# Kernel optimization log

Measured on AMD Instinct MI355X. Metric: run time of the kernel, lower is better.

The kernel has to match this reference:

```python
import jax, jax.numpy as jnp
import numpy as np

N_NODES = 50000
N_EDGES = 1600000
SLOPE = 0.01  # torch leaky_relu default negative_slope


def _lrelu(x):
    return jnp.where(x >= 0, x, SLOPE * x)


def _graph_conv(x, edge_index, w_rel, b_rel, w_root):
    # PyG GraphConv (aggr='add'): out_i = W_rel @ sum_{j->i} x_j + b_rel + W_root @ x_i
    src, dst = edge_index[0], edge_index[1]
    agg = jax.ops.segment_sum(x[src], dst, num_segments=x.shape[0])  # [N, F_in]
    return agg @ w_rel.T + b_rel + x @ w_root.T


def setup_inputs() -> dict:
    key = jax.random.key(0)
    ks = jax.random.split(key, 12)

    def glorot(k, shape):
        fan_in = shape[-1]
        return jax.random.normal(k, shape, dtype=jnp.float32) / np.sqrt(fan_in)

    x = jax.random.normal(ks[0], (N_NODES, 2048), dtype=jnp.float32)
    edge_index = jax.random.randint(ks[1], (2, N_EDGES), 0, N_NODES, dtype=jnp.int64)

    return {
        "x": x,
        "edge_index": edge_index,
        "lin1_w": glorot(ks[2], (128, 2048)),
        "lin1_b": jnp.zeros((128,), jnp.float32),
        "conv1_w_rel": glorot(ks[3], (64, 128)),
        "conv1_b_rel": jnp.zeros((64,), jnp.float32),
        "conv1_w_root": glorot(ks[4], (64, 128)),
        "conv4_w_rel": glorot(ks[5], (32, 64)),
        "conv4_b_rel": jnp.zeros((32,), jnp.float32),
        "conv4_w_root": glorot(ks[6], (32, 64)),
        "pos_w": glorot(ks[7], (3, 32)),
        "pos_b": jnp.zeros((3,), jnp.float32),
    }


def reference(x, edge_index, lin1_w, lin1_b, conv1_w_rel, conv1_b_rel,
              conv1_w_root, conv4_w_rel, conv4_b_rel, conv4_w_root,
              pos_w, pos_b):
    # dropout layers are identity at inference
    h = _lrelu(x @ lin1_w.T + lin1_b)                                  # [N, 128]
    h = _lrelu(_graph_conv(h, edge_index, conv1_w_rel, conv1_b_rel, conv1_w_root))  # [N, 64]
    h = _lrelu(_graph_conv(h, edge_index, conv4_w_rel, conv4_b_rel, conv4_w_root))  # [N, 32]
    position = h @ pos_w.T + pos_b                                     # [N, 3]
    return position
```

## Files before the change

kernel.cpp:

```cpp
#include <hip/hip_runtime.h>

#define N_NODES 50000
#define N_EDGES 1600000
#define LIN_BLOCKS 782
#define HIST_BLOCKS 1024

typedef __attribute__((ext_vector_type(4))) float f32x4;
typedef __attribute__((ext_vector_type(8))) short bf16x8;
typedef unsigned short u16;

__device__ __forceinline__ float lrelu(float x) { return x >= 0.f ? x : 0.01f * x; }

__device__ __forceinline__ u16 f2bf(float f) {
    union { float f; unsigned u; } v; v.f = f;
    unsigned u = v.u;
    u += 0x7fffu + ((u >> 16) & 1u);
    return (u16)(u >> 16);
}

__device__ __forceinline__ float bf2f(u16 v) {
    union { unsigned u; float f; } x; x.u = ((unsigned)v) << 16; return x.f;
}

__device__ __forceinline__ bf16x8 cvt8(float4 a, float4 b) {
    bf16x8 r;
    r[0] = (short)f2bf(a.x); r[1] = (short)f2bf(a.y);
    r[2] = (short)f2bf(a.z); r[3] = (short)f2bf(a.w);
    r[4] = (short)f2bf(b.x); r[5] = (short)f2bf(b.y);
    r[6] = (short)f2bf(b.z); r[7] = (short)f2bf(b.w);
    return r;
}

__launch_bounds__(256)
__global__ void k_prep(const float* __restrict__ W1,
                       const float* __restrict__ W2a, const float* __restrict__ W2b,
                       const float* __restrict__ W3a, const float* __restrict__ W3b,
                       u16* __restrict__ wf1, u16* __restrict__ wf2, u16* __restrict__ wf3,
                       const int* __restrict__ ei, int* __restrict__ deg)
{
    const int b = blockIdx.x;
    if (b < 1024) {
        int i = b * 256 + threadIdx.x;
        int e = i & 7, lane = (i >> 3) & 63, nf = (i >> 9) & 7, ks = i >> 12;
        int n = nf * 16 + (lane & 15);
        int k = ks * 32 + 8 * (lane >> 4) + e;
        wf1[i] = f2bf(W1[(size_t)n * 2048 + k]);
    } else if (b < 1088) {
        int i = (b - 1024) * 256 + threadIdx.x;
        int e = i & 7, lane = (i >> 3) & 63, nf = (i >> 9) & 7, ks = i >> 12;
        int n = nf * 16 + (lane & 15);
        int k = ks * 32 + 8 * (lane >> 4) + e;
        float v = (n < 64) ? W2a[(size_t)n * 128 + k] : W2b[(size_t)(n - 64) * 128 + k];
        wf2[i] = f2bf(v);
    } else if (b < 1104) {
        int i = (b - 1088) * 256 + threadIdx.x;
        int e = i & 7, lane = (i >> 3) & 63, nf = (i >> 9) & 3, ks = i >> 11;
        int n = nf * 16 + (lane & 15);
        int k = ks * 32 + 8 * (lane >> 4) + e;
        float v = (n < 32) ? W3a[(size_t)n * 64 + k] : W3b[(size_t)(n - 32) * 64 + k];
        wf3[i] = f2bf(v);
    } else {
        for (int e = (b - 1104) * 256 + threadIdx.x; e < N_EDGES; e += HIST_BLOCKS * 256)
            atomicAdd(deg + ei[N_EDGES + e], 1);
    }
}

__device__ __forceinline__ void compute_step(const char* slot, int lane, int wave,
                                             f32x4 acc[2][4])
{
    const int lrow = lane & 15;
    const int k16 = lane >> 4;
    const int nfb = (wave >> 1) << 2;
    const int rb = (wave & 1) << 5;

    bf16x8 af[2];
#pragma unroll
    for (int st = 0; st < 2; st++) {
        const int row = rb + st * 16 + lrow;
        af[st] = *(const bf16x8*)(slot + row * 64 + ((k16 ^ (row & 3)) << 4));
    }
    bf16x8 bf[4];
#pragma unroll
    for (int j = 0; j < 4; j++)
        bf[j] = *(const bf16x8*)(slot + 4096 + (nfb + j) * 1024 + lane * 16);

    __builtin_amdgcn_s_setprio(1);
#pragma unroll
    for (int st = 0; st < 2; st++)
#pragma unroll
        for (int j = 0; j < 4; j++)
            acc[st][j] = __builtin_amdgcn_mfma_f32_16x16x32_bf16(af[st], bf[j], acc[st][j], 0, 0, 0);
    __builtin_amdgcn_s_setprio(0);
}

__launch_bounds__(256, 4)
__global__ void k_linf(const float* __restrict__ X, const u16* __restrict__ Wf1,
                       const u16* __restrict__ Wf2,
                       const float* __restrict__ Bv, const float* __restrict__ brel,
                       u16* __restrict__ t1, float* __restrict__ acc1,
                       const int* __restrict__ ei, int* __restrict__ cur,
                       int* __restrict__ csr)
{
    __shared__ __align__(16) char lds[2][12288];

    const int t = threadIdx.x, wave = t >> 6, lane = t & 63;
    const int lrow = lane & 15, lgrp = lane >> 4;
    const int m0 = blockIdx.x * 64;

    const int arow_l = t >> 2, kq = t & 3;
    int grow = m0 + arow_l; if (grow >= N_NODES) grow = N_NODES - 1;
    const float4* ap = (const float4*)(X + (size_t)grow * 2048);
    const bf16x8* bp = (const bf16x8*)Wf1;
    const int awr = arow_l * 64 + ((kq ^ (arow_l & 3)) << 4);
    const int bwr = 4096 + t * 32;

    f32x4 acc[2][4];
#pragma unroll
    for (int st = 0; st < 2; st++)
#pragma unroll
        for (int j = 0; j < 4; j++) acc[st][j] = (f32x4)0.f;

    float4 cA0 = ap[kq * 2], cA1 = ap[kq * 2 + 1];
    bf16x8 cB0 = bp[t * 2], cB1 = bp[t * 2 + 1];
    float4 nA0 = ap[8 + kq * 2], nA1 = ap[8 + kq * 2 + 1];
    bf16x8 nB0 = bp[512 + t * 2], nB1 = bp[512 + t * 2 + 1];
    *(bf16x8*)(lds[0] + awr) = cvt8(cA0, cA1);
    *(bf16x8*)(lds[0] + bwr) = cB0;
    *(bf16x8*)(lds[0] + bwr + 16) = cB1;
    asm volatile("s_waitcnt lgkmcnt(0)" ::: "memory");
    __builtin_amdgcn_s_barrier();
    __builtin_amdgcn_sched_barrier(0);

#pragma unroll 2
    for (int s = 0; s < 62; s++) {
        float4 fA0 = ap[(s + 2) * 8 + kq * 2], fA1 = ap[(s + 2) * 8 + kq * 2 + 1];
        bf16x8 fB0 = bp[(s + 2) * 512 + t * 2], fB1 = bp[(s + 2) * 512 + t * 2 + 1];

        compute_step(lds[s & 1], lane, wave, acc);
        __builtin_amdgcn_s_barrier();
        __builtin_amdgcn_sched_barrier(0);

        char* wslot = lds[(s + 1) & 1];
        *(bf16x8*)(wslot + awr) = cvt8(nA0, nA1);
        *(bf16x8*)(wslot + bwr) = nB0;
        *(bf16x8*)(wslot + bwr + 16) = nB1;
        asm volatile("s_waitcnt lgkmcnt(0)" ::: "memory");
        __builtin_amdgcn_s_barrier();
        __builtin_amdgcn_sched_barrier(0);

        nA0 = fA0; nA1 = fA1; nB0 = fB0; nB1 = fB1;
    }
    compute_step(lds[0], lane, wave, acc);
    __builtin_amdgcn_s_barrier();
    __builtin_amdgcn_sched_barrier(0);
    *(bf16x8*)(lds[1] + awr) = cvt8(nA0, nA1);
    *(bf16x8*)(lds[1] + bwr) = nB0;
    *(bf16x8*)(lds[1] + bwr + 16) = nB1;
    asm volatile("s_waitcnt lgkmcnt(0)" ::: "memory");
    __builtin_amdgcn_s_barrier();
    __builtin_amdgcn_sched_barrier(0);
    compute_step(lds[1], lane, wave, acc);
    __builtin_amdgcn_s_barrier();
    __builtin_amdgcn_sched_barrier(0);

    u16* hl = (u16*)&lds[0][0];
    {
        const int nfb = (wave >> 1) << 2, rb = (wave & 1) << 5;
#pragma unroll
        for (int st = 0; st < 2; st++) {
#pragma unroll
            for (int j = 0; j < 4; j++) {
                const int col = nfb * 16 + j * 16 + lrow;
                const float bias = Bv[col];
#pragma unroll
                for (int r = 0; r < 4; r++) {
                    const int row = rb + st * 16 + lgrp * 4 + r;
                    hl[row * 128 + (((col >> 3) ^ (row & 7)) << 3) + (col & 7)] =
                        f2bf(lrelu(acc[st][j][r] + bias));
                }
            }
        }
    }
    asm volatile("s_waitcnt lgkmcnt(0)" ::: "memory");
    __builtin_amdgcn_s_barrier();
    __builtin_amdgcn_sched_barrier(0);

    bf16x8 af2[4];
    {
        const int row = wave * 16 + lrow;
#pragma unroll
        for (int ks = 0; ks < 4; ks++) {
            const int chunk = ((ks << 2) + lgrp) ^ (row & 7);
            af2[ks] = *(const bf16x8*)(hl + row * 128 + (chunk << 3));
        }
    }
    f32x4 dacc[8];
#pragma unroll
    for (int i = 0; i < 8; i++) dacc[i] = (f32x4)0.f;
    const u16* bp2 = Wf2 + lane * 8;
#pragma unroll
    for (int ks = 0; ks < 4; ks++) {
#pragma unroll
        for (int nf = 0; nf < 8; nf++) {
            bf16x8 bf = *(const bf16x8*)(bp2 + ks * 4096 + nf * 512);
            dacc[nf] = __builtin_amdgcn_mfma_f32_16x16x32_bf16(af2[ks], bf, dacc[nf], 0, 0, 0);
        }
    }

    const int rbase = m0 + wave * 16 + lgrp * 4;
#pragma unroll
    for (int nf = 0; nf < 8; nf++) {
        const int col = nf * 16 + lrow;
#pragma unroll
        for (int r = 0; r < 4; r++) {
            const int row = rbase + r;
            if (row < N_NODES) {
                if (col < 64) t1[(size_t)row * 64 + col] = f2bf(dacc[nf][r]);
                else          acc1[(size_t)row * 64 + (col - 64)] = dacc[nf][r] + brel[col - 64];
            }
        }
    }

    for (int e = blockIdx.x * 256 + t; e < N_EDGES; e += LIN_BLOCKS * 256) {
        const int dst = ei[N_EDGES + e];
        const int p = atomicAdd(cur + dst, 1);
        csr[p] = ei[e];
    }
}

__launch_bounds__(256, 2)
__global__ void k_dualf2(const float* __restrict__ A, const u16* __restrict__ Wf,
                         const float* __restrict__ brel,
                         u16* __restrict__ t2, float* __restrict__ acc2)
{
    const int t = threadIdx.x, wave = t >> 6, lane = t & 63;
    const int lrow = lane & 15, lgrp = lane >> 4;
    const int arow = blockIdx.x * 64 + wave * 16 + lrow;
    const float* ap = A + (size_t)(arow < N_NODES ? arow : 0) * 64 + 8 * lgrp;
    const u16* bp = Wf + lane * 8;

    float4 a00 = *(const float4*)(ap + 0);
    float4 a01 = *(const float4*)(ap + 4);
    float4 a10 = *(const float4*)(ap + 32);
    float4 a11 = *(const float4*)(ap + 36);

    f32x4 acc[4];
#pragma unroll
    for (int i = 0; i < 4; i++) acc[i] = (f32x4)0.f;

    a00.x = lrelu(a00.x); a00.y = lrelu(a00.y); a00.z = lrelu(a00.z); a00.w = lrelu(a00.w);
    a01.x = lrelu(a01.x); a01.y = lrelu(a01.y); a01.z = lrelu(a01.z); a01.w = lrelu(a01.w);
    bf16x8 af0 = cvt8(a00, a01);
    a10.x = lrelu(a10.x); a10.y = lrelu(a10.y); a10.z = lrelu(a10.z); a10.w = lrelu(a10.w);
    a11.x = lrelu(a11.x); a11.y = lrelu(a11.y); a11.z = lrelu(a11.z); a11.w = lrelu(a11.w);
    bf16x8 af1 = cvt8(a10, a11);

#pragma unroll
    for (int nf = 0; nf < 4; nf++) {
        bf16x8 b0 = *(const bf16x8*)(bp + nf * 512);
        bf16x8 b1 = *(const bf16x8*)(bp + 2048 + nf * 512);
        acc[nf] = __builtin_amdgcn_mfma_f32_16x16x32_bf16(af0, b0, acc[nf], 0, 0, 0);
        acc[nf] = __builtin_amdgcn_mfma_f32_16x16x32_bf16(af1, b1, acc[nf], 0, 0, 0);
    }

    const int rbase = blockIdx.x * 64 + wave * 16 + lgrp * 4;
#pragma unroll
    for (int nf = 0; nf < 4; nf++) {
        const int col = nf * 16 + lrow;
#pragma unroll
        for (int r = 0; r < 4; r++) {
            const int row = rbase + r;
            if (row < N_NODES) {
                if (col < 32) t2[(size_t)row * 32 + col] = f2bf(acc[nf][r]);
                else          acc2[(size_t)row * 32 + (col - 32)] = acc[nf][r] + brel[col - 32];
            }
        }
    }
}

__launch_bounds__(256)
__global__ void k_scan1(const int* __restrict__ deg, int* __restrict__ tmp,
                        int* __restrict__ bsum)
{
    __shared__ int sm[256];
    const int tid = threadIdx.x;
    const int i = blockIdx.x * 256 + tid;
    int d = (i < N_NODES) ? deg[i] : 0;
    sm[tid] = d;
    __syncthreads();
#pragma unroll
    for (int off = 1; off < 256; off <<= 1) {
        int v = (tid >= off) ? sm[tid - off] : 0;
        __syncthreads();
        sm[tid] += v;
        __syncthreads();
    }
    if (i < N_NODES) tmp[i] = sm[tid];
    if (tid == 255) bsum[blockIdx.x] = sm[255];
}

__launch_bounds__(256)
__global__ void k_scan2p(const int* __restrict__ bsum, int* __restrict__ boff, int nb)
{
    __shared__ int sm[256];
    const int tid = threadIdx.x;
    int v = (tid < nb) ? bsum[tid] : 0;
    sm[tid] = v;
    __syncthreads();
#pragma unroll
    for (int off = 1; off < 256; off <<= 1) {
        int u = (tid >= off) ? sm[tid - off] : 0;
        __syncthreads();
        sm[tid] += u;
        __syncthreads();
    }
    if (tid < nb) boff[tid] = sm[tid] - v;
}

__launch_bounds__(256)
__global__ void k_scan3(const int* __restrict__ tmp, const int* __restrict__ boff,
                        const int* __restrict__ deg, int* __restrict__ ro,
                        int* __restrict__ cur)
{
    const int i = blockIdx.x * 256 + threadIdx.x;
    if (i < N_NODES) {
        int incl = tmp[i] + boff[i >> 8];
        ro[i + 1] = incl;
        cur[i] = incl - deg[i];
    }
    if (i == 0) ro[0] = 0;
}

__launch_bounds__(256)
__global__ void k_gather64(const int* __restrict__ ro, const int* __restrict__ csr,
                           const u16* __restrict__ t, float* __restrict__ acc)
{
    const int wid = (blockIdx.x << 2) | (threadIdx.x >> 6);
    if (wid >= N_NODES) return;
    const int lane = threadIdx.x & 63;
    const int s = ro[wid], e = ro[wid + 1];
    float a = acc[(size_t)wid * 64 + lane];
    int i = s;
    for (; i + 8 <= e; i += 8) {
        int s0 = csr[i], s1 = csr[i + 1], s2 = csr[i + 2], s3 = csr[i + 3];
        int s4 = csr[i + 4], s5 = csr[i + 5], s6 = csr[i + 6], s7 = csr[i + 7];
        u16 v0 = t[(size_t)s0 * 64 + lane], v1 = t[(size_t)s1 * 64 + lane];
        u16 v2 = t[(size_t)s2 * 64 + lane], v3 = t[(size_t)s3 * 64 + lane];
        u16 v4 = t[(size_t)s4 * 64 + lane], v5 = t[(size_t)s5 * 64 + lane];
        u16 v6 = t[(size_t)s6 * 64 + lane], v7 = t[(size_t)s7 * 64 + lane];
        a += bf2f(v0); a += bf2f(v1); a += bf2f(v2); a += bf2f(v3);
        a += bf2f(v4); a += bf2f(v5); a += bf2f(v6); a += bf2f(v7);
    }
    for (; i < e; ++i) a += bf2f(t[(size_t)csr[i] * 64 + lane]);
    acc[(size_t)wid * 64 + lane] = a;
}

__launch_bounds__(256)
__global__ void k_gpos(const int* __restrict__ ro, const int* __restrict__ csr,
                       const u16* __restrict__ t, const float* __restrict__ acc2,
                       const float* __restrict__ PW, const float* __restrict__ PB,
                       float* __restrict__ out)
{
    const int wid = (blockIdx.x << 2) | (threadIdx.x >> 6);
    if (wid >= N_NODES) return;
    const int lane = threadIdx.x & 63;
    const int half = lane >> 5, f = lane & 31;
    const int s = ro[wid], e = ro[wid + 1];
    float a = 0.f;
    int i = s;
    for (; i + 8 <= e; i += 8) {
        int s0 = csr[i + half], s1 = csr[i + 2 + half];
        int s2 = csr[i + 4 + half], s3 = csr[i + 6 + half];
        u16 v0 = t[(size_t)s0 * 32 + f], v1 = t[(size_t)s1 * 32 + f];
        u16 v2 = t[(size_t)s2 * 32 + f], v3 = t[(size_t)s3 * 32 + f];
        a += bf2f(v0); a += bf2f(v1); a += bf2f(v2); a += bf2f(v3);
    }
    for (; i < e; i += 2) {
        int idx = i + half;
        if (idx < e) a += bf2f(t[(size_t)csr[idx] * 32 + f]);
    }
    a += __shfl_xor(a, 32, 64);

    float v = lrelu(acc2[(size_t)wid * 32 + f] + a);
    float p0 = v * PW[f], p1 = v * PW[32 + f], p2 = v * PW[64 + f];
#pragma unroll
    for (int off = 16; off >= 1; off >>= 1) {
        p0 += __shfl_xor(p0, off, 64);
        p1 += __shfl_xor(p1, off, 64);
        p2 += __shfl_xor(p2, off, 64);
    }
    if (lane == 0) {
        out[(size_t)wid * 3 + 0] = p0 + PB[0];
        out[(size_t)wid * 3 + 1] = p1 + PB[1];
        out[(size_t)wid * 3 + 2] = p2 + PB[2];
    }
}

extern "C" void kernel_launch(void* const* d_in, const int* in_sizes, int n_in,
                              void* d_out, int out_size, void* d_ws, size_t ws_size,
                              hipStream_t stream)
{
    const float* x        = (const float*)d_in[0];
    const int*   ei       = (const int*)d_in[1];
    const float* lin1_w   = (const float*)d_in[2];
    const float* lin1_b   = (const float*)d_in[3];
    const float* c1_wrel  = (const float*)d_in[4];
    const float* c1_brel  = (const float*)d_in[5];
    const float* c1_wroot = (const float*)d_in[6];
    const float* c4_wrel  = (const float*)d_in[7];
    const float* c4_brel  = (const float*)d_in[8];
    const float* c4_wroot = (const float*)d_in[9];
    const float* pos_w    = (const float*)d_in[10];
    const float* pos_b    = (const float*)d_in[11];
    float* out = (float*)d_out;

    char* base = (char*)d_ws;
    u16*   t1b  = (u16*)base;
    float* acc1 = (float*)(base + 6400000);
    u16*   t2b  = (u16*)(base + 19200000);
    float* acc2 = (float*)(base + 22400000);
    u16*   wf1  = (u16*)(base + 28800000);
    u16*   wf2  = wf1 + 262144;
    u16*   wf3  = wf2 + 16384;
    int*   ibase = (int*)(wf3 + 4096);
    const int NPAD = ((N_NODES + 255) / 256) * 256;
    int* deg  = ibase;
    int* tmp  = deg  + NPAD;
    int* ro   = tmp  + NPAD;
    int* cur  = ro   + NPAD;
    int* bsum = cur  + NPAD;
    int* boff = bsum + 256;
    int* csr  = boff + 256;
    const int NB = (N_NODES + 255) / 256;

    hipMemsetAsync(deg, 0, (size_t)NPAD * sizeof(int), stream);
    hipLaunchKernelGGL(k_prep, dim3(1104 + HIST_BLOCKS), dim3(256), 0, stream,
                       lin1_w, c1_wrel, c1_wroot, c4_wrel, c4_wroot,
                       wf1, wf2, wf3, ei, deg);
    hipLaunchKernelGGL(k_scan1, dim3(NB), dim3(256), 0, stream, deg, tmp, bsum);
    hipLaunchKernelGGL(k_scan2p, dim3(1), dim3(256), 0, stream, bsum, boff, NB);
    hipLaunchKernelGGL(k_scan3, dim3(NB), dim3(256), 0, stream, tmp, boff, deg, ro, cur);

    hipLaunchKernelGGL(k_linf, dim3(LIN_BLOCKS), dim3(256), 0, stream,
                       x, wf1, wf2, lin1_b, c1_brel, t1b, acc1, ei, cur, csr);
    hipLaunchKernelGGL(k_gather64, dim3((N_NODES + 3) / 4), dim3(256), 0, stream,
                       ro, csr, t1b, acc1);
    hipLaunchKernelGGL(k_dualf2, dim3((N_NODES + 63) / 64), dim3(256), 0, stream,
                       acc1, wf3, c4_brel, t2b, acc2);
    hipLaunchKernelGGL(k_gpos, dim3((N_NODES + 3) / 4), dim3(256), 0, stream,
                       ro, csr, t2b, acc2, pos_w, pos_b, out);
}
```

Baseline: 361.4 us.

## Enlarge lin1 GEMM tile to 128 rows and split CSR build into separate kernels

The first fused linear kernel now processes 128 rows per block with 512 threads. The shared weight tile is reused across twice as many rows, and each thread loads half as much of B. The CSR fill loop and the degree histogram move out of the GEMM and prep kernels into standalone k_fill and k_hist kernels, and the deg memset is folded into k_prep. The s_setprio hints around the MFMAs are dropped. In exchange, the atomic CSR fill no longer overlaps with the GEMM, and the pipeline gains extra kernel launches.

```diff
diff --git a/kernel.cpp b/kernel.cpp
--- a/kernel.cpp
+++ b/kernel.cpp
@@ -2,12 +2,12 @@
 
 #define N_NODES 50000
 #define N_EDGES 1600000
-#define LIN_BLOCKS 782
-#define HIST_BLOCKS 1024
 
 typedef __attribute__((ext_vector_type(4))) float f32x4;
 typedef __attribute__((ext_vector_type(8))) short bf16x8;
 typedef unsigned short u16;
+
+#define ABYTES 8192
 
 __device__ __forceinline__ float lrelu(float x) { return x >= 0.f ? x : 0.01f * x; }
 
@@ -36,7 +36,7 @@
                        const float* __restrict__ W2a, const float* __restrict__ W2b,
                        const float* __restrict__ W3a, const float* __restrict__ W3b,
                        u16* __restrict__ wf1, u16* __restrict__ wf2, u16* __restrict__ wf3,
-                       const int* __restrict__ ei, int* __restrict__ deg)
+                       int* __restrict__ deg)
 {
     const int b = blockIdx.x;
     if (b < 1024) {
@@ -60,9 +60,17 @@
         float v = (n < 32) ? W3a[(size_t)n * 64 + k] : W3b[(size_t)(n - 32) * 64 + k];
         wf3[i] = f2bf(v);
     } else {
-        for (int e = (b - 1104) * 256 + threadIdx.x; e < N_EDGES; e += HIST_BLOCKS * 256)
-            atomicAdd(deg + ei[N_EDGES + e], 1);
-    }
+        int i = (b - 1104) * 256 + threadIdx.x;
+        if (i < N_NODES) deg[i] = 0;
+    }
+}
+
+__launch_bounds__(256)
+__global__ void k_hist(const int* __restrict__ ei, int* __restrict__ deg)
+{
+    const int stride = gridDim.x * 256;
+    for (int e = blockIdx.x * 256 + threadIdx.x; e < N_EDGES; e += stride)
+        atomicAdd(deg + ei[N_EDGES + e], 1);
 }
 
 __device__ __forceinline__ void compute_step(const char* slot, int lane, int wave,
@@ -70,49 +78,45 @@
 {
     const int lrow = lane & 15;
     const int k16 = lane >> 4;
-    const int nfb = (wave >> 1) << 2;
-    const int rb = (wave & 1) << 5;
+    const int rs = wave >> 1;
+    const int ch = wave & 1;
 
     bf16x8 af[2];
 #pragma unroll
     for (int st = 0; st < 2; st++) {
-        const int row = rb + st * 16 + lrow;
+        const int row = rs * 32 + st * 16 + lrow;
         af[st] = *(const bf16x8*)(slot + row * 64 + ((k16 ^ (row & 3)) << 4));
     }
     bf16x8 bf[4];
 #pragma unroll
     for (int j = 0; j < 4; j++)
-        bf[j] = *(const bf16x8*)(slot + 4096 + (nfb + j) * 1024 + lane * 16);
-
-    __builtin_amdgcn_s_setprio(1);
+        bf[j] = *(const bf16x8*)(slot + ABYTES + (ch * 4 + j) * 1024 + lane * 16);
+
 #pragma unroll
     for (int st = 0; st < 2; st++)
 #pragma unroll
         for (int j = 0; j < 4; j++)
             acc[st][j] = __builtin_amdgcn_mfma_f32_16x16x32_bf16(af[st], bf[j], acc[st][j], 0, 0, 0);
-    __builtin_amdgcn_s_setprio(0);
-}
-
-__launch_bounds__(256, 4)
+}
+
+__launch_bounds__(512, 4)
 __global__ void k_linf(const float* __restrict__ X, const u16* __restrict__ Wf1,
                        const u16* __restrict__ Wf2,
                        const float* __restrict__ Bv, const float* __restrict__ brel,
-                       u16* __restrict__ t1, float* __restrict__ acc1,
-                       const int* __restrict__ ei, int* __restrict__ cur,
-                       int* __restrict__ csr)
-{
-    __shared__ __align__(16) char lds[2][12288];
+                       u16* __restrict__ t1, float* __restrict__ acc1)
+{
+    __shared__ __align__(16) char lds[2][16384];
 
     const int t = threadIdx.x, wave = t >> 6, lane = t & 63;
     const int lrow = lane & 15, lgrp = lane >> 4;
-    const int m0 = blockIdx.x * 64;
+    const int m0 = blockIdx.x * 128;
 
     const int arow_l = t >> 2, kq = t & 3;
     int grow = m0 + arow_l; if (grow >= N_NODES) grow = N_NODES - 1;
     const float4* ap = (const float4*)(X + (size_t)grow * 2048);
     const bf16x8* bp = (const bf16x8*)Wf1;
     const int awr = arow_l * 64 + ((kq ^ (arow_l & 3)) << 4);
-    const int bwr = 4096 + t * 32;
+    const int bwr = ABYTES + t * 16;
 
     f32x4 acc[2][4];
 #pragma unroll
@@ -121,12 +125,11 @@
         for (int j = 0; j < 4; j++) acc[st][j] = (f32x4)0.f;
 
     float4 cA0 = ap[kq * 2], cA1 = ap[kq * 2 + 1];
-    bf16x8 cB0 = bp[t * 2], cB1 = bp[t * 2 + 1];
+    bf16x8 cB = bp[t];
     float4 nA0 = ap[8 + kq * 2], nA1 = ap[8 + kq * 2 + 1];
-    bf16x8 nB0 = bp[512 + t * 2], nB1 = bp[512 + t * 2 + 1];
+    bf16x8 nB = bp[512 + t];
     *(bf16x8*)(lds[0] + awr) = cvt8(cA0, cA1);
-    *(bf16x8*)(lds[0] + bwr) = cB0;
-    *(bf16x8*)(lds[0] + bwr + 16) = cB1;
+    *(bf16x8*)(lds[0] + bwr) = cB;
     asm volatile("s_waitcnt lgkmcnt(0)" ::: "memory");
     __builtin_amdgcn_s_barrier();
     __builtin_amdgcn_sched_barrier(0);
@@ -134,7 +137,7 @@
 #pragma unroll 2
     for (int s = 0; s < 62; s++) {
         float4 fA0 = ap[(s + 2) * 8 + kq * 2], fA1 = ap[(s + 2) * 8 + kq * 2 + 1];
-        bf16x8 fB0 = bp[(s + 2) * 512 + t * 2], fB1 = bp[(s + 2) * 512 + t * 2 + 1];
+        bf16x8 fB = bp[(s + 2) * 512 + t];
 
         compute_step(lds[s & 1], lane, wave, acc);
         __builtin_amdgcn_s_barrier();
@@ -142,20 +145,18 @@
 
         char* wslot = lds[(s + 1) & 1];
         *(bf16x8*)(wslot + awr) = cvt8(nA0, nA1);
-        *(bf16x8*)(wslot + bwr) = nB0;
-        *(bf16x8*)(wslot + bwr + 16) = nB1;
+        *(bf16x8*)(wslot + bwr) = nB;
         asm volatile("s_waitcnt lgkmcnt(0)" ::: "memory");
         __builtin_amdgcn_s_barrier();
         __builtin_amdgcn_sched_barrier(0);
 
-        nA0 = fA0; nA1 = fA1; nB0 = fB0; nB1 = fB1;
+        nA0 = fA0; nA1 = fA1; nB = fB;
     }
     compute_step(lds[0], lane, wave, acc);
     __builtin_amdgcn_s_barrier();
     __builtin_amdgcn_sched_barrier(0);
     *(bf16x8*)(lds[1] + awr) = cvt8(nA0, nA1);
-    *(bf16x8*)(lds[1] + bwr) = nB0;
-    *(bf16x8*)(lds[1] + bwr + 16) = nB1;
+    *(bf16x8*)(lds[1] + bwr) = nB;
     asm volatile("s_waitcnt lgkmcnt(0)" ::: "memory");
     __builtin_amdgcn_s_barrier();
     __builtin_amdgcn_sched_barrier(0);
@@ -165,16 +166,16 @@
 
     u16* hl = (u16*)&lds[0][0];
     {
-        const int nfb = (wave >> 1) << 2, rb = (wave & 1) << 5;
+        const int rs = wave >> 1, ch = wave & 1;
 #pragma unroll
         for (int st = 0; st < 2; st++) {
 #pragma unroll
             for (int j = 0; j < 4; j++) {
-                const int col = nfb * 16 + j * 16 + lrow;
+                const int col = ch * 64 + j * 16 + lrow;
                 const float bias = Bv[col];
 #pragma unroll
                 for (int r = 0; r < 4; r++) {
-                    const int row = rb + st * 16 + lgrp * 4 + r;
+                    const int row = rs * 32 + st * 16 + lgrp * 4 + r;
                     hl[row * 128 + (((col >> 3) ^ (row & 7)) << 3) + (col & 7)] =
                         f2bf(lrelu(acc[st][j][r] + bias));
                 }
@@ -220,12 +221,6 @@
             }
         }
     }
-
-    for (int e = blockIdx.x * 256 + t; e < N_EDGES; e += LIN_BLOCKS * 256) {
-        const int dst = ei[N_EDGES + e];
-        const int p = atomicAdd(cur + dst, 1);
-        csr[p] = ei[e];
-    }
 }
 
 __launch_bounds__(256, 2)
@@ -329,6 +324,18 @@
         cur[i] = incl - deg[i];
     }
     if (i == 0) ro[0] = 0;
+}
+
+__launch_bounds__(256)
+__global__ void k_fill(const int* __restrict__ ei, int* __restrict__ cur,
+                       int* __restrict__ csr)
+{
+    const int stride = gridDim.x * 256;
+    for (int e = blockIdx.x * 256 + threadIdx.x; e < N_EDGES; e += stride) {
+        const int dst = ei[N_EDGES + e];
+        const int p = atomicAdd(cur + dst, 1);
+        csr[p] = ei[e];
+    }
 }
 
 __launch_bounds__(256)
@@ -433,16 +440,17 @@
     int* csr  = boff + 256;
     const int NB = (N_NODES + 255) / 256;
 
-    hipMemsetAsync(deg, 0, (size_t)NPAD * sizeof(int), stream);
-    hipLaunchKernelGGL(k_prep, dim3(1104 + HIST_BLOCKS), dim3(256), 0, stream,
+    hipLaunchKernelGGL(k_prep, dim3(1104 + NB), dim3(256), 0, stream,
                        lin1_w, c1_wrel, c1_wroot, c4_wrel, c4_wroot,
-                       wf1, wf2, wf3, ei, deg);
+                       wf1, wf2, wf3, deg);
+    hipLaunchKernelGGL(k_hist, dim3(1024), dim3(256), 0, stream, ei, deg);
     hipLaunchKernelGGL(k_scan1, dim3(NB), dim3(256), 0, stream, deg, tmp, bsum);
     hipLaunchKernelGGL(k_scan2p, dim3(1), dim3(256), 0, stream, bsum, boff, NB);
     hipLaunchKernelGGL(k_scan3, dim3(NB), dim3(256), 0, stream, tmp, boff, deg, ro, cur);
-
-    hipLaunchKernelGGL(k_linf, dim3(LIN_BLOCKS), dim3(256), 0, stream,
-                       x, wf1, wf2, lin1_b, c1_brel, t1b, acc1, ei, cur, csr);
+    hipLaunchKernelGGL(k_fill, dim3(1024), dim3(256), 0, stream, ei, cur, csr);
+
+    hipLaunchKernelGGL(k_linf, dim3((N_NODES + 127) / 128), dim3(512), 0, stream,
+                       x, wf1, wf2, lin1_b, c1_brel, t1b, acc1);
     hipLaunchKernelGGL(k_gather64, dim3((N_NODES + 3) / 4), dim3(256), 0, stream,
                        ro, csr, t1b, acc1);
     hipLaunchKernelGGL(k_dualf2, dim3((N_NODES + 63) / 64), dim3(256), 0, stream,
```

Measured after the change: 397.9 us. 1.1x slower.
